# Performance work log

Measured on AMD Instinct MI355X. Metric: run time of the kernel, lower is better.

## Reference

```python
import jax, jax.numpy as jnp
import numpy as np

N_FRAMES = 100000
HIDDEN = 512
N_QUERIES = 256
N_EVENTS = 2048
TOPK = 8
FRAME_RATE = 5.0
EPS = 1e-12


def setup_inputs() -> dict:
    key = jax.random.key(0)
    k1, k2, k3, k4 = jax.random.split(key, 4)
    video_feats = jax.random.normal(k1, (1, N_FRAMES, HIDDEN), dtype=jnp.float32)
    query_feats = jax.random.normal(k2, (N_QUERIES, HIDDEN), dtype=jnp.float32)
    video_events = jnp.sort(
        jax.random.randint(k3, (N_FRAMES,), 0, N_EVENTS, dtype=jnp.int32))
    W_reg = jax.random.normal(k4, (HIDDEN, 2), dtype=jnp.float32) * 0.02
    b_reg = jnp.zeros((2,), dtype=jnp.float32)
    return {"video_feats": video_feats, "query_feats": query_feats,
            "video_events": video_events, "W_reg": W_reg, "b_reg": b_reg}


def reference(video_feats, query_feats, video_events, W_reg, b_reg):
    vf = video_feats[0]                                   # [N, D]
    n = vf.shape[0]
    # --- per-event masked-mean pooling (segment mean) ---
    sums = jax.ops.segment_sum(vf, video_events, num_segments=N_EVENTS)          # [E, D]
    counts = jax.ops.segment_sum(jnp.ones((n,), vf.dtype), video_events,
                                 num_segments=N_EVENTS)                          # [E]
    event_avg = sums / jnp.maximum(counts, 1.0)[:, None]                         # [E, D]
    # --- event timestamps: first/last frame index per event / frame_rate ---
    idx = jnp.arange(n, dtype=jnp.int32)
    start = jax.ops.segment_min(idx, video_events, num_segments=N_EVENTS)
    end = jax.ops.segment_max(idx, video_events, num_segments=N_EVENTS)
    # empty events get int extremes; zero them out (they have zero features anyway)
    nonempty = counts > 0
    start = jnp.where(nonempty, start, 0)
    end = jnp.where(nonempty, end, 0)
    event_ts = jnp.stack([start, end], axis=-1).astype(jnp.float32) / FRAME_RATE  # [E, 2]
    # --- cosine similarity query x event ---
    qn = query_feats / jnp.maximum(
        jnp.linalg.norm(query_feats, axis=-1, keepdims=True), EPS)
    en = event_avg / jnp.maximum(
        jnp.linalg.norm(event_avg, axis=-1, keepdims=True), EPS)
    sim = qn @ en.T                                       # [Q, E]
    # --- per-query top-k event selection ---
    _, top_idx = jax.lax.top_k(sim, TOPK)                 # [Q, K]
    sel_ts = event_ts[top_idx]                            # [Q, K, 2]
    sel_dur = sel_ts[..., 1] - sel_ts[..., 0]             # [Q, K]
    sel_feat = event_avg[top_idx]                         # [Q, K, D]
    interact = sel_feat * query_feats[:, None, :]         # [Q, K, D]
    bbox_bias = jnp.tanh(jnp.einsum('qkd,dt->qkt', interact, W_reg) + b_reg)  # [Q, K, 2]
    pred_timestamps = sel_ts + bbox_bias * sel_dur[..., None]
    return pred_timestamps
```

## Files before the change

### kernel.cpp

```cpp
#include <hip/hip_runtime.h>
#include <hip/hip_bf16.h>
#include <math.h>

#define N_FRAMES 100000
#define HIDDEN 512
#define N_QUERIES 256
#define N_EVENTS 2048
#define TOPK 8
#define FRAME_RATE 5.0f
#define EPSN 1e-12f


__global__ void initq_k(const float* __restrict__ qf, float* __restrict__ inv_qn,
                        int* __restrict__ start, int* __restrict__ end) {
    int blk = blockIdx.x;
    int lane = threadIdx.x;
    if (blk < N_QUERIES) {
        const float* row = qf + (size_t)blk * HIDDEN;
        float ss = 0.f;
        #pragma unroll
        for (int i = 0; i < 8; ++i) { float v = row[lane + 64 * i]; ss += v * v; }
        #pragma unroll
        for (int off = 32; off; off >>= 1) ss += __shfl_xor(ss, off);
        if (lane == 0) inv_qn[blk] = 1.0f / fmaxf(sqrtf(ss), EPSN);
    } else {
        int e = (blk - N_QUERIES) * 64 + lane;
        start[e] = -1; end[e] = -1;
    }
}

__global__ void bounds_k(const int* __restrict__ ev, int* __restrict__ start,
                         int* __restrict__ end) {
    int i = blockIdx.x * blockDim.x + threadIdx.x;
    if (i >= N_FRAMES) return;
    int e = ev[i];
    if (i == 0 || ev[i - 1] != e) start[e] = i;
    if (i == N_FRAMES - 1 || ev[i + 1] != e) end[e] = i;
}

__global__ void pool_k(const float* __restrict__ vf, const int* __restrict__ start,
                       const int* __restrict__ end, float* __restrict__ avg,
                       float* __restrict__ inv_en, float* __restrict__ ts) {
    int e = blockIdx.x;
    int s = start[e], t = end[e];
    int tid = threadIdx.x;
    int half = tid >> 7;
    int l = tid & 127;
    float4 acc = make_float4(0.f, 0.f, 0.f, 0.f);
    if (s >= 0) {
        const float4* p = (const float4*)vf + (size_t)(s + half) * 128 + l;
        int f = s + half;
        for (; f + 2 <= t; f += 4, p += 512) {
            float4 v0 = p[0];
            float4 v1 = p[256];
            acc.x += v0.x + v1.x; acc.y += v0.y + v1.y;
            acc.z += v0.z + v1.z; acc.w += v0.w + v1.w;
        }
        if (f <= t) {
            float4 v0 = *p;
            acc.x += v0.x; acc.y += v0.y; acc.z += v0.z; acc.w += v0.w;
        }
    }
    __shared__ float4 buf[128];
    __shared__ float ssbuf[2];
    if (half) buf[l] = acc;
    __syncthreads();
    if (!half) {
        float4 o = buf[l];
        acc.x += o.x; acc.y += o.y; acc.z += o.z; acc.w += o.w;
        if (s >= 0) {
            float cnt = (float)(t - s + 1);
            acc.x /= cnt; acc.y /= cnt; acc.z /= cnt; acc.w /= cnt;
        }
        *((float4*)avg + (size_t)e * 128 + l) = acc;
        float ss = acc.x * acc.x + acc.y * acc.y + acc.z * acc.z + acc.w * acc.w;
        #pragma unroll
        for (int off = 32; off; off >>= 1) ss += __shfl_xor(ss, off);
        if ((tid & 63) == 0) ssbuf[tid >> 6] = ss;
    }
    __syncthreads();
    if (tid == 0) {
        float ss = ssbuf[0] + ssbuf[1];
        inv_en[e] = (s >= 0) ? 1.0f / fmaxf(sqrtf(ss), EPSN) : 0.0f;
        ts[e * 2 + 0] = (s >= 0) ? (float)s / FRAME_RATE : 0.0f;
        ts[e * 2 + 1] = (s >= 0) ? (float)t / FRAME_RATE : 0.0f;
    }
}

#define BQ 64
#define BE 32
#define DC 128
#define DCP 132
#define KSPLIT 2
#define KHALF (HIDDEN / KSPLIT)

__global__ void sim_k(const float* __restrict__ qf, const float* __restrict__ avg,
                      float* __restrict__ part) {
    __shared__ float qs[BQ][DCP];
    __shared__ float es[BE][DCP];
    int tid = threadIdx.x;
    int qbase = blockIdx.y * BQ;
    int ebase = blockIdx.x * BE;
    int kb = blockIdx.z;
    int q0 = tid >> 3;
    int e0 = tid & 7;
    float acc[4][4] = {{0.f,0.f,0.f,0.f},{0.f,0.f,0.f,0.f},
                       {0.f,0.f,0.f,0.f},{0.f,0.f,0.f,0.f}};
    for (int dcl = 0; dcl < KHALF; dcl += DC) {
        int dc = kb * KHALF + dcl;
        __syncthreads();
        #pragma unroll
        for (int r = 0; r < 16; ++r) {
            int ldx = tid + 128 * r;
            int row = ldx >> 5, c4 = ldx & 31;
            *(float4*)&qs[row][c4 * 4] =
                *(const float4*)(qf + (size_t)(qbase + row) * HIDDEN + dc + c4 * 4);
        }
        #pragma unroll
        for (int r = 0; r < 8; ++r) {
            int ldx = tid + 128 * r;
            int row = ldx >> 5, c4 = ldx & 31;
            *(float4*)&es[row][c4 * 4] =
                *(const float4*)(avg + (size_t)(ebase + row) * HIDDEN + dc + c4 * 4);
        }
        __syncthreads();
        #pragma unroll 2
        for (int d = 0; d < DC; d += 4) {
            float4 ev0 = *(const float4*)&es[e0][d];
            float4 ev1 = *(const float4*)&es[e0 + 8][d];
            float4 ev2 = *(const float4*)&es[e0 + 16][d];
            float4 ev3 = *(const float4*)&es[e0 + 24][d];
            #pragma unroll
            for (int i = 0; i < 4; ++i) {
                float4 qv = *(const float4*)&qs[q0 + 16 * i][d];
                acc[i][0] += qv.x * ev0.x + qv.y * ev0.y + qv.z * ev0.z + qv.w * ev0.w;
                acc[i][1] += qv.x * ev1.x + qv.y * ev1.y + qv.z * ev1.z + qv.w * ev1.w;
                acc[i][2] += qv.x * ev2.x + qv.y * ev2.y + qv.z * ev2.z + qv.w * ev2.w;
                acc[i][3] += qv.x * ev3.x + qv.y * ev3.y + qv.z * ev3.z + qv.w * ev3.w;
            }
        }
    }
    float* pk = part + (size_t)kb * N_QUERIES * N_EVENTS;
    #pragma unroll
    for (int i = 0; i < 4; ++i) {
        size_t rowoff = (size_t)(qbase + q0 + 16 * i) * N_EVENTS + ebase;
        #pragma unroll
        for (int j = 0; j < 4; ++j)
            pk[rowoff + e0 + 8 * j] = acc[i][j];
    }
}

__global__ void topk_final_k(const float* __restrict__ part, const float* __restrict__ inv_en,
                             const float* __restrict__ inv_qn, const float* __restrict__ ts,
                             const float* __restrict__ avg, const float* __restrict__ qf,
                             const float* __restrict__ W, const float* __restrict__ b,
                             float* __restrict__ out) {
    int q = blockIdx.x;
    int lane = threadIdx.x;
    const float4* r0 = (const float4*)(part + (size_t)q * N_EVENTS);
    const float4* r1 = (const float4*)(part + (size_t)N_QUERIES * N_EVENTS + (size_t)q * N_EVENTS);
    const float4* ie4 = (const float4*)inv_en;
    float iq = inv_qn[q];
    float4 v4[8];
    #pragma unroll
    for (int g = 0; g < 8; ++g) {
        float4 a = r0[lane + 64 * g];
        float4 c = r1[lane + 64 * g];
        float4 e = ie4[lane + 64 * g];
        v4[g].x = (a.x + c.x) * e.x * iq;
        v4[g].y = (a.y + c.y) * e.y * iq;
        v4[g].z = (a.z + c.z) * e.z * iq;
        v4[g].w = (a.w + c.w) * e.w * iq;
    }
    int chosen[TOPK];
    #pragma unroll
    for (int k = 0; k < TOPK; ++k) {
        float best = -INFINITY;
        int bidx = 0x7fffffff;
        #pragma unroll
        for (int g = 0; g < 8; ++g) {
            #pragma unroll
            for (int j = 0; j < 4; ++j) {
                int idx = 4 * lane + 256 * g + j;
                float val = (j == 0) ? v4[g].x : (j == 1) ? v4[g].y
                          : (j == 2) ? v4[g].z : v4[g].w;
                bool dup = false;
                #pragma unroll
                for (int m = 0; m < TOPK; ++m)
                    dup = dup || ((m < k) && (chosen[m] == idx));
                if (!dup && val > best) { best = val; bidx = idx; }
            }
        }
        #pragma unroll
        for (int off = 32; off; off >>= 1) {
            float ov = __shfl_xor(best, off);
            int oi = __shfl_xor(bidx, off);
            if (ov > best || (ov == best && oi < bidx)) { best = ov; bidx = oi; }
        }
        chosen[k] = bidx;
    }
    const float* qrow = qf + (size_t)q * HIDDEN;
    float qreg[8];
    float2 wreg[8];
    #pragma unroll
    for (int i = 0; i < 8; ++i) qreg[i] = qrow[lane + 64 * i];
    #pragma unroll
    for (int i = 0; i < 8; ++i) wreg[i] = ((const float2*)W)[lane + 64 * i];
    float b0s = b[0], b1s = b[1];
    #pragma unroll
    for (int k = 0; k < TOPK; ++k) {
        int e = chosen[k];
        const float* frow = avg + (size_t)e * HIDDEN;
        float a0 = 0.f, a1 = 0.f;
        #pragma unroll
        for (int i = 0; i < 8; ++i) {
            float f = frow[lane + 64 * i] * qreg[i];
            a0 += f * wreg[i].x;
            a1 += f * wreg[i].y;
        }
        #pragma unroll
        for (int off = 32; off; off >>= 1) {
            a0 += __shfl_xor(a0, off);
            a1 += __shfl_xor(a1, off);
        }
        if (lane == 0) {
            float t0 = ts[e * 2 + 0], t1 = ts[e * 2 + 1];
            float dur = t1 - t0;
            out[(q * TOPK + k) * 2 + 0] = t0 + tanhf(a0 + b0s) * dur;
            out[(q * TOPK + k) * 2 + 1] = t1 + tanhf(a1 + b1s) * dur;
        }
    }
}

extern "C" void kernel_launch(void* const* d_in, const int* in_sizes, int n_in,
                              void* d_out, int out_size, void* d_ws, size_t ws_size,
                              hipStream_t stream) {
    const float* vf = (const float*)d_in[0];
    const float* qf = (const float*)d_in[1];
    const int* ev = (const int*)d_in[2];
    const float* W = (const float*)d_in[3];
    const float* b = (const float*)d_in[4];
    float* out = (float*)d_out;

    char* ws = (char*)d_ws;
    float* avg    = (float*)(ws + 0);
    float* ts     = (float*)(ws + 4194304);
    float* inv_en = (float*)(ws + 4210688);
    float* inv_qn = (float*)(ws + 4218880);
    int*   start  = (int*)  (ws + 4219904);
    int*   endp   = (int*)  (ws + 4228096);
    float* part   = (float*)(ws + 4236288);

    initq_k<<<N_QUERIES + N_EVENTS / 64, 64, 0, stream>>>(qf, inv_qn, start, endp);
    bounds_k<<<(N_FRAMES + 255) / 256, 256, 0, stream>>>(ev, start, endp);
    pool_k<<<N_EVENTS, 256, 0, stream>>>(vf, start, endp, avg, inv_en, ts);
    dim3 sgrid(N_EVENTS / BE, N_QUERIES / BQ, KSPLIT);
    sim_k<<<sgrid, 128, 0, stream>>>(qf, avg, part);
    topk_final_k<<<N_QUERIES, 64, 0, stream>>>(part, inv_en, inv_qn, ts, avg, qf, W, b, out);
}
```

Baseline: 340.4 us.

## Replace bounds kernels with binary search in pool and fold query norm into topk

Removes the init and bounds kernels. Each pool block now finds its event range with two binary searches over the sorted event array, and the query norm is computed inside the top-k kernel from registers it already loads. This cuts two kernel launches and the scattered start/end writes. In exchange, every pool block does about 17 dependent global loads per search before streaming features, and the code now relies on the events being sorted.

```diff
diff --git a/kernel.cpp b/kernel.cpp
--- a/kernel.cpp
+++ b/kernel.cpp
@@ -11,43 +11,28 @@
 #define EPSN 1e-12f
 
 
-__global__ void initq_k(const float* __restrict__ qf, float* __restrict__ inv_qn,
-                        int* __restrict__ start, int* __restrict__ end) {
-    int blk = blockIdx.x;
-    int lane = threadIdx.x;
-    if (blk < N_QUERIES) {
-        const float* row = qf + (size_t)blk * HIDDEN;
-        float ss = 0.f;
-        #pragma unroll
-        for (int i = 0; i < 8; ++i) { float v = row[lane + 64 * i]; ss += v * v; }
-        #pragma unroll
-        for (int off = 32; off; off >>= 1) ss += __shfl_xor(ss, off);
-        if (lane == 0) inv_qn[blk] = 1.0f / fmaxf(sqrtf(ss), EPSN);
-    } else {
-        int e = (blk - N_QUERIES) * 64 + lane;
-        start[e] = -1; end[e] = -1;
-    }
-}
-
-__global__ void bounds_k(const int* __restrict__ ev, int* __restrict__ start,
-                         int* __restrict__ end) {
-    int i = blockIdx.x * blockDim.x + threadIdx.x;
-    if (i >= N_FRAMES) return;
-    int e = ev[i];
-    if (i == 0 || ev[i - 1] != e) start[e] = i;
-    if (i == N_FRAMES - 1 || ev[i + 1] != e) end[e] = i;
-}
-
-__global__ void pool_k(const float* __restrict__ vf, const int* __restrict__ start,
-                       const int* __restrict__ end, float* __restrict__ avg,
-                       float* __restrict__ inv_en, float* __restrict__ ts) {
+__device__ __forceinline__ int lower_bound_ev(const int* __restrict__ ev, int val) {
+    int lo = 0, hi = N_FRAMES;
+    while (lo < hi) {
+        int mid = (lo + hi) >> 1;
+        if (ev[mid] < val) lo = mid + 1; else hi = mid;
+    }
+    return lo;
+}
+
+__global__ void pool_k(const float* __restrict__ vf, const int* __restrict__ ev,
+                       float* __restrict__ avg, float* __restrict__ inv_en,
+                       float* __restrict__ ts) {
     int e = blockIdx.x;
-    int s = start[e], t = end[e];
+    int s = lower_bound_ev(ev, e);
+    int e_end = lower_bound_ev(ev, e + 1);
+    int t = e_end - 1;
+    bool nonempty = e_end > s;
     int tid = threadIdx.x;
     int half = tid >> 7;
     int l = tid & 127;
     float4 acc = make_float4(0.f, 0.f, 0.f, 0.f);
-    if (s >= 0) {
+    if (nonempty) {
         const float4* p = (const float4*)vf + (size_t)(s + half) * 128 + l;
         int f = s + half;
         for (; f + 2 <= t; f += 4, p += 512) {
@@ -68,7 +53,7 @@
     if (!half) {
         float4 o = buf[l];
         acc.x += o.x; acc.y += o.y; acc.z += o.z; acc.w += o.w;
-        if (s >= 0) {
+        if (nonempty) {
             float cnt = (float)(t - s + 1);
             acc.x /= cnt; acc.y /= cnt; acc.z /= cnt; acc.w /= cnt;
         }
@@ -81,9 +66,9 @@
     __syncthreads();
     if (tid == 0) {
         float ss = ssbuf[0] + ssbuf[1];
-        inv_en[e] = (s >= 0) ? 1.0f / fmaxf(sqrtf(ss), EPSN) : 0.0f;
-        ts[e * 2 + 0] = (s >= 0) ? (float)s / FRAME_RATE : 0.0f;
-        ts[e * 2 + 1] = (s >= 0) ? (float)t / FRAME_RATE : 0.0f;
+        inv_en[e] = nonempty ? 1.0f / fmaxf(sqrtf(ss), EPSN) : 0.0f;
+        ts[e * 2 + 0] = nonempty ? (float)s / FRAME_RATE : 0.0f;
+        ts[e * 2 + 1] = nonempty ? (float)t / FRAME_RATE : 0.0f;
     }
 }
 
@@ -151,16 +136,25 @@
 }
 
 __global__ void topk_final_k(const float* __restrict__ part, const float* __restrict__ inv_en,
-                             const float* __restrict__ inv_qn, const float* __restrict__ ts,
-                             const float* __restrict__ avg, const float* __restrict__ qf,
-                             const float* __restrict__ W, const float* __restrict__ b,
-                             float* __restrict__ out) {
+                             const float* __restrict__ ts, const float* __restrict__ avg,
+                             const float* __restrict__ qf, const float* __restrict__ W,
+                             const float* __restrict__ b, float* __restrict__ out) {
     int q = blockIdx.x;
     int lane = threadIdx.x;
+    const float* qrow = qf + (size_t)q * HIDDEN;
+    float qreg[8];
+    #pragma unroll
+    for (int i = 0; i < 8; ++i) qreg[i] = qrow[lane + 64 * i];
+    float ss = 0.f;
+    #pragma unroll
+    for (int i = 0; i < 8; ++i) ss += qreg[i] * qreg[i];
+    #pragma unroll
+    for (int off = 32; off; off >>= 1) ss += __shfl_xor(ss, off);
+    float iq = 1.0f / fmaxf(sqrtf(ss), EPSN);
+
     const float4* r0 = (const float4*)(part + (size_t)q * N_EVENTS);
     const float4* r1 = (const float4*)(part + (size_t)N_QUERIES * N_EVENTS + (size_t)q * N_EVENTS);
     const float4* ie4 = (const float4*)inv_en;
-    float iq = inv_qn[q];
     float4 v4[8];
     #pragma unroll
     for (int g = 0; g < 8; ++g) {
@@ -199,11 +193,7 @@
         }
         chosen[k] = bidx;
     }
-    const float* qrow = qf + (size_t)q * HIDDEN;
-    float qreg[8];
     float2 wreg[8];
-    #pragma unroll
-    for (int i = 0; i < 8; ++i) qreg[i] = qrow[lane + 64 * i];
     #pragma unroll
     for (int i = 0; i < 8; ++i) wreg[i] = ((const float2*)W)[lane + 64 * i];
     float b0s = b[0], b1s = b[1];
@@ -246,15 +236,10 @@
     float* avg    = (float*)(ws + 0);
     float* ts     = (float*)(ws + 4194304);
     float* inv_en = (float*)(ws + 4210688);
-    float* inv_qn = (float*)(ws + 4218880);
-    int*   start  = (int*)  (ws + 4219904);
-    int*   endp   = (int*)  (ws + 4228096);
     float* part   = (float*)(ws + 4236288);
 
-    initq_k<<<N_QUERIES + N_EVENTS / 64, 64, 0, stream>>>(qf, inv_qn, start, endp);
-    bounds_k<<<(N_FRAMES + 255) / 256, 256, 0, stream>>>(ev, start, endp);
-    pool_k<<<N_EVENTS, 256, 0, stream>>>(vf, start, endp, avg, inv_en, ts);
+    pool_k<<<N_EVENTS, 256, 0, stream>>>(vf, ev, avg, inv_en, ts);
     dim3 sgrid(N_EVENTS / BE, N_QUERIES / BQ, KSPLIT);
     sim_k<<<sgrid, 128, 0, stream>>>(qf, avg, part);
-    topk_final_k<<<N_QUERIES, 64, 0, stream>>>(part, inv_en, inv_qn, ts, avg, qf, W, b, out);
-}
+    topk_final_k<<<N_QUERIES, 64, 0, stream>>>(part, inv_en, ts, avg, qf, W, b, out);
+}
```

After: 342.8 us. Within noise of the previous version (+0.7%).
